# Kernel tuning notes

Hardware: AMD Instinct MI355X
Metric: run time of the kernel (lower is better)

Reference implementation:

```python
import math
import jax, jax.numpy as jnp
import numpy as np

B, T, E = 1, 4096, 768
H, D = 12, 64
RA_WINDOW = 512
INIT_GATES = (2.2, 0.6, 0.1)


def setup_inputs() -> dict:
    key = jax.random.key(0)
    ks = jax.random.split(key, 6)
    x = jax.random.normal(ks[0], (B, T, E), dtype=jnp.float32)
    # Linear weights stored as [in, out] (math-equivalent to torch's x @ W.T)
    s = 1.0 / math.sqrt(E)
    Wq = jax.random.normal(ks[1], (E, H * D), dtype=jnp.float32) * s
    Wk = jax.random.normal(ks[2], (E, H * D), dtype=jnp.float32) * s
    Wv = jax.random.normal(ks[3], (E, H * D), dtype=jnp.float32) * s
    Wo = jax.random.normal(ks[4], (H * D, E), dtype=jnp.float32) * s
    gates = jnp.tile(jnp.asarray(INIT_GATES, dtype=jnp.float32)[None, :], (H, 1))  # [H,3]
    u = jax.random.normal(ks[5], (H, D), dtype=jnp.float32) * 0.02
    return {"x": x, "Wq": Wq, "Wk": Wk, "Wv": Wv, "Wo": Wo, "gates": gates, "u": u}


def reference(x, Wq, Wk, Wv, Wo, gates, u):
    # projections -> [B,H,T,D]
    def proj(W):
        return (x @ W).reshape(B, T, H, D).transpose(0, 2, 1, 3)
    Q, K, V = proj(Wq), proj(Wk), proj(Wv)

    S = jnp.einsum('bhtd,bhsd->bhts', Q, K) / math.sqrt(D)  # [B,H,T,T]

    w = jax.nn.softmax(gates, axis=-1)  # [H,3]
    w_std = w[:, 0][None, :, None, None]
    w_rec = w[:, 1][None, :, None, None]
    w_disc = w[:, 2][None, :, None, None]

    logits = w_std * S + w_rec * jnp.swapaxes(S, -2, -1)

    # discoverability column bias from K via per-head u
    d_raw = jnp.einsum('bhtd,hd->bht', K, u)
    d = d_raw - jnp.mean(d_raw, axis=-1, keepdims=True)
    logits = logits + w_disc * d[:, :, None, :]

    # causal banded mask
    idx = jnp.arange(T)
    mask = (idx[None, :] <= idx[:, None]) & (jnp.abs(idx[None, :] - idx[:, None]) <= RA_WINDOW)
    logits = jnp.where(mask[None, None, :, :], logits, -jnp.inf)

    attn = jax.nn.softmax(logits, axis=-1)
    ctx = jnp.einsum('bhts,bhsd->bhtd', attn, V)
    out = ctx.transpose(0, 2, 1, 3).reshape(B, T, H * D) @ Wo
    return (out, attn)
```

## Files before the change

### kernel.cpp

```cpp
#include <hip/hip_runtime.h>
#include <cstddef>

#define T_LEN 4096
#define EMB 768
#define NH 12
#define HD 64
#define WIN 512
#define PBW 640

#define GBM 128
#define GBN 128
#define GBK 16

__global__ __launch_bounds__(256) void gemm3_f32(const float* __restrict__ A,
                                                 const float* __restrict__ B0,
                                                 const float* __restrict__ B1,
                                                 const float* __restrict__ B2,
                                                 float* __restrict__ C0,
                                                 float* __restrict__ C1,
                                                 float* __restrict__ C2,
                                                 int M, int N, int K) {
    __shared__ float As[GBK][GBM + 4];
    __shared__ float Bs[GBK][GBN + 4];
    const int tid = threadIdx.x;
    const int bm = blockIdx.y * GBM;
    const int bn = blockIdx.x * GBN;
    const float* __restrict__ B = (blockIdx.z == 0) ? B0 : (blockIdx.z == 1) ? B1 : B2;
    float* __restrict__ C = (blockIdx.z == 0) ? C0 : (blockIdx.z == 1) ? C1 : C2;

    const int ty = (tid >> 4) << 2;
    const int tx = (tid & 15) << 2;

    const int ar = tid >> 1;
    const int ac = (tid & 1) << 3;
    const int br = tid >> 4;
    const int bc = (tid & 15) << 3;

    float acc[8][8] = {};

    float4 pa0 = *(const float4*)&A[(size_t)(bm + ar) * K + ac];
    float4 pa1 = *(const float4*)&A[(size_t)(bm + ar) * K + ac + 4];
    float4 pb0 = *(const float4*)&B[(size_t)br * N + bn + bc];
    float4 pb1 = *(const float4*)&B[(size_t)br * N + bn + bc + 4];

    for (int k0 = 0; k0 < K; k0 += GBK) {
        As[ac + 0][ar] = pa0.x; As[ac + 1][ar] = pa0.y; As[ac + 2][ar] = pa0.z; As[ac + 3][ar] = pa0.w;
        As[ac + 4][ar] = pa1.x; As[ac + 5][ar] = pa1.y; As[ac + 6][ar] = pa1.z; As[ac + 7][ar] = pa1.w;
        *(float4*)&Bs[br][bc]     = pb0;
        *(float4*)&Bs[br][bc + 4] = pb1;
        __syncthreads();
        if (k0 + GBK < K) {
            pa0 = *(const float4*)&A[(size_t)(bm + ar) * K + k0 + GBK + ac];
            pa1 = *(const float4*)&A[(size_t)(bm + ar) * K + k0 + GBK + ac + 4];
            pb0 = *(const float4*)&B[(size_t)(k0 + GBK + br) * N + bn + bc];
            pb1 = *(const float4*)&B[(size_t)(k0 + GBK + br) * N + bn + bc + 4];
        }
#pragma unroll
        for (int k = 0; k < GBK; ++k) {
            const float4 a0v = *(const float4*)&As[k][ty];
            const float4 a1v = *(const float4*)&As[k][ty + 64];
            const float4 b0v = *(const float4*)&Bs[k][tx];
            const float4 b1v = *(const float4*)&Bs[k][tx + 64];
            const float av[8] = {a0v.x, a0v.y, a0v.z, a0v.w, a1v.x, a1v.y, a1v.z, a1v.w};
            const float bv[8] = {b0v.x, b0v.y, b0v.z, b0v.w, b1v.x, b1v.y, b1v.z, b1v.w};
#pragma unroll
            for (int i = 0; i < 8; ++i)
#pragma unroll
                for (int j = 0; j < 8; ++j)
                    acc[i][j] += av[i] * bv[j];
        }
        __syncthreads();
    }
#pragma unroll
    for (int i = 0; i < 8; ++i) {
        const int r = bm + ty + ((i < 4) ? i : (60 + i));
        *(float4*)&C[(size_t)r * N + bn + tx]      = make_float4(acc[i][0], acc[i][1], acc[i][2], acc[i][3]);
        *(float4*)&C[(size_t)r * N + bn + tx + 64] = make_float4(acc[i][4], acc[i][5], acc[i][6], acc[i][7]);
    }
}

__global__ __launch_bounds__(256) void dbias_kernel(const float* __restrict__ K,
                                                    const float* __restrict__ u,
                                                    float* __restrict__ d_bias) {
    const int h = blockIdx.x;
    const int tid = threadIdx.x;
    __shared__ __align__(16) float us[HD];
    __shared__ float dr[T_LEN];
    __shared__ float red[256];
    if (tid < HD) us[tid] = u[h * HD + tid];
    __syncthreads();
    const float4* u4 = (const float4*)us;
    float lsum = 0.f;
    for (int t = tid; t < T_LEN; t += 256) {
        const float4* Kp = (const float4*)&K[(size_t)t * EMB + h * HD];
        float acc = 0.f;
#pragma unroll
        for (int i = 0; i < HD / 4; ++i) {
            float4 k4 = Kp[i];
            float4 uu = u4[i];
            acc += k4.x * uu.x + k4.y * uu.y + k4.z * uu.z + k4.w * uu.w;
        }
        dr[t] = acc;
        lsum += acc;
    }
    red[tid] = lsum;
    __syncthreads();
    for (int off = 128; off > 0; off >>= 1) {
        if (tid < off) red[tid] += red[tid + off];
        __syncthreads();
    }
    const float mean = red[0] * (1.0f / (float)T_LEN);
    __syncthreads();
    for (int t = tid; t < T_LEN; t += 256) {
        d_bias[h * T_LEN + t] = dr[t] - mean;
    }
}

__global__ __launch_bounds__(256) void attn_band_kernel(const float* __restrict__ Q,
                                                        const float* __restrict__ K,
                                                        const float* __restrict__ V,
                                                        const float* __restrict__ d_bias,
                                                        const float* __restrict__ gates,
                                                        float* __restrict__ Pb,
                                                        float* __restrict__ Fb,
                                                        float* __restrict__ ctx) {
    const int t0  = blockIdx.x << 6;
    const int h   = blockIdx.y;
    const int tid = threadIdx.x;
    const int cg  = tid & 15;
    const int tm  = (tid >> 4) << 2;
    const int tn4 = cg << 2;

    const int lm = tid >> 2;
    const int lk = (tid & 3) << 4;
    const int sr = tid >> 1;
    const int sc = (tid & 1) << 5;

    __shared__ __align__(16) float QT[64][68];
    __shared__ __align__(16) float KT[64][68];
    __shared__ __align__(16) float Bc[64][136];
    __shared__ float cmf[5][64];
    __shared__ float rmf[64], idvf[64];
    float* __restrict__ Bp = &Bc[0][0];

    const float g0 = gates[h * 3 + 0];
    const float g1 = gates[h * 3 + 1];
    const float g2 = gates[h * 3 + 2];
    const float gm = fmaxf(g0, fmaxf(g1, g2));
    const float e0 = __expf(g0 - gm), e1 = __expf(g1 - gm), e2 = __expf(g2 - gm);
    const float gi = 1.0f / (e0 + e1 + e2);
    const float w_std = e0 * gi * 0.125f;
    const float w_rec = e1 * gi * 0.125f;
    const float w_disc = e2 * gi;

    const int cp_start = (t0 >= 576) ? 0 : ((576 - t0) >> 7);
    int s0 = t0 - 576 + (cp_start << 7);

    float4 kr[8], qr[8];
    {
        int srow = s0 + sr; srow = srow < 0 ? 0 : srow;
        const float* Kp = K + (size_t)srow * EMB + h * HD + sc;
#pragma unroll
        for (int c = 0; c < 8; ++c) kr[c] = *(const float4*)(Kp + 4 * c);
    }

    {
        const float* Qp = Q + (size_t)(t0 + lm) * EMB + h * HD + lk;
        const float* Kp = K + (size_t)(t0 + lm) * EMB + h * HD + lk;
#pragma unroll
        for (int it = 0; it < 4; ++it) {
            float4 a = *(const float4*)(Qp + 4 * it);
            QT[lk + 4 * it + 0][lm] = a.x;
            QT[lk + 4 * it + 1][lm] = a.y;
            QT[lk + 4 * it + 2][lm] = a.z;
            QT[lk + 4 * it + 3][lm] = a.w;
            float4 b = *(const float4*)(Kp + 4 * it);
            KT[lk + 4 * it + 0][lm] = b.x;
            KT[lk + 4 * it + 1][lm] = b.y;
            KT[lk + 4 * it + 2][lm] = b.z;
            KT[lk + 4 * it + 3][lm] = b.w;
        }
    }

    float rm[4], rden[4], acc[4][4];
#pragma unroll
    for (int i = 0; i < 4; ++i) {
        rm[i] = -1e30f;
        rden[i] = 0.f;
#pragma unroll
        for (int j = 0; j < 4; ++j) acc[i][j] = 0.f;
    }

    for (int cp = cp_start; cp < 5; ++cp) {
        __syncthreads();
#pragma unroll
        for (int c = 0; c < 8; ++c) {
            Bc[sc + 4 * c + 0][sr] = kr[c].x;
            Bc[sc + 4 * c + 1][sr] = kr[c].y;
            Bc[sc + 4 * c + 2][sr] = kr[c].z;
            Bc[sc + 4 * c + 3][sr] = kr[c].w;
        }
        __syncthreads();

        {
            int srow = s0 + sr; srow = srow < 0 ? 0 : srow;
            const float* Qp = Q + (size_t)srow * EMB + h * HD + sc;
#pragma unroll
            for (int c = 0; c < 8; ++c) qr[c] = *(const float4*)(Qp + 4 * c);
        }

        float m1[4][8] = {};
#pragma unroll 8
        for (int k = 0; k < 64; ++k) {
            const float4 a4 = *(const float4*)&QT[k][tm];
            const float4 b0 = *(const float4*)&Bc[k][tn4];
            const float4 b1 = *(const float4*)&Bc[k][tn4 + 64];
            const float av[4] = {a4.x, a4.y, a4.z, a4.w};
            const float bv[8] = {b0.x, b0.y, b0.z, b0.w, b1.x, b1.y, b1.z, b1.w};
#pragma unroll
            for (int i = 0; i < 4; ++i)
#pragma unroll
                for (int j = 0; j < 8; ++j)
                    m1[i][j] += av[i] * bv[j];
        }
        __syncthreads();

#pragma unroll
        for (int c = 0; c < 8; ++c) {
            Bc[sc + 4 * c + 0][sr] = qr[c].x;
            Bc[sc + 4 * c + 1][sr] = qr[c].y;
            Bc[sc + 4 * c + 2][sr] = qr[c].z;
            Bc[sc + 4 * c + 3][sr] = qr[c].w;
        }
        __syncthreads();

        if (cp < 4) {
            int srow = s0 + 128 + sr; srow = srow < 0 ? 0 : srow;
            const float* Kp = K + (size_t)srow * EMB + h * HD + sc;
#pragma unroll
            for (int c = 0; c < 8; ++c) kr[c] = *(const float4*)(Kp + 4 * c);
        }

        float m2[4][8] = {};
#pragma unroll 8
        for (int k = 0; k < 64; ++k) {
            const float4 a4 = *(const float4*)&KT[k][tm];
            const float4 b0 = *(const float4*)&Bc[k][tn4];
            const float4 b1 = *(const float4*)&Bc[k][tn4 + 64];
            const float av[4] = {a4.x, a4.y, a4.z, a4.w};
            const float bv[8] = {b0.x, b0.y, b0.z, b0.w, b1.x, b1.y, b1.z, b1.w};
#pragma unroll
            for (int i = 0; i < 4; ++i)
#pragma unroll
                for (int j = 0; j < 8; ++j)
                    m2[i][j] += av[i] * bv[j];
        }

        const int i0 = s0 + tn4;
        const int i0c = i0 < 0 ? 0 : i0;
        const float4 db0 = *(const float4*)&d_bias[h * T_LEN + i0c];
        const float4 db1 = *(const float4*)&d_bias[h * T_LEN + s0 + 64 + tn4];
        const float dbv[8] = {db0.x, db0.y, db0.z, db0.w, db1.x, db1.y, db1.z, db1.w};
        float l[4][8];
#pragma unroll
        for (int i = 0; i < 4; ++i) {
            const int t = t0 + tm + i;
#pragma unroll
            for (int j = 0; j < 8; ++j) {
                const int s = s0 + ((j < 4) ? (tn4 + j) : (tn4 + j + 60));
                const float lv = w_std * m1[i][j] + w_rec * m2[i][j] + w_disc * dbv[j];
                const bool valid = (s >= 0) && (s <= t) && (s >= t - WIN);
                l[i][j] = valid ? lv : -1e30f;
            }
        }
#pragma unroll
        for (int i = 0; i < 4; ++i) {
            float cmx = fmaxf(fmaxf(fmaxf(l[i][0], l[i][1]), fmaxf(l[i][2], l[i][3])),
                              fmaxf(fmaxf(l[i][4], l[i][5]), fmaxf(l[i][6], l[i][7])));
#pragma unroll
            for (int off = 1; off < 16; off <<= 1) cmx = fmaxf(cmx, __shfl_xor(cmx, off));
            const float nm = fmaxf(rm[i], cmx);
            const float f = __expf(rm[i] - nm);
            float cs = 0.f;
#pragma unroll
            for (int j = 0; j < 8; ++j) {
                const float p = __expf(l[i][j] - nm);
                l[i][j] = p;
                cs += p;
            }
#pragma unroll
            for (int off = 1; off < 16; off <<= 1) cs += __shfl_xor(cs, off);
            rden[i] = rden[i] * f + cs;
            rm[i] = nm;
#pragma unroll
            for (int j = 0; j < 4; ++j) acc[i][j] *= f;
            if (cg == 0) cmf[cp][tm + i] = nm;
            float* prow = &Pb[((size_t)(h * T_LEN + t0 + tm + i)) * PBW + (cp << 7)];
            *(float4*)&prow[tn4]      = make_float4(l[i][0], l[i][1], l[i][2], l[i][3]);
            *(float4*)&prow[64 + tn4] = make_float4(l[i][4], l[i][5], l[i][6], l[i][7]);
        }
        __syncthreads();

#pragma unroll
        for (int j = 0; j < 4; ++j) {
            *(float4*)&Bp[(tn4 + j) * 68 + tm] =
                make_float4(l[0][j], l[1][j], l[2][j], l[3][j]);
            *(float4*)&Bp[(tn4 + j + 64) * 68 + tm] =
                make_float4(l[0][j + 4], l[1][j + 4], l[2][j + 4], l[3][j + 4]);
        }
        __syncthreads();

#pragma unroll 8
        for (int k = 0; k < 128; ++k) {
            const float4 av = *(const float4*)&Bp[k * 68 + tm];
            int vrow = s0 + k; vrow = vrow < 0 ? 0 : vrow;
            const float4 bv = *(const float4*)&V[(size_t)vrow * EMB + h * HD + tn4];
            acc[0][0] += av.x * bv.x; acc[0][1] += av.x * bv.y; acc[0][2] += av.x * bv.z; acc[0][3] += av.x * bv.w;
            acc[1][0] += av.y * bv.x; acc[1][1] += av.y * bv.y; acc[1][2] += av.y * bv.z; acc[1][3] += av.y * bv.w;
            acc[2][0] += av.z * bv.x; acc[2][1] += av.z * bv.y; acc[2][2] += av.z * bv.z; acc[2][3] += av.z * bv.w;
            acc[3][0] += av.w * bv.x; acc[3][1] += av.w * bv.y; acc[3][2] += av.w * bv.z; acc[3][3] += av.w * bv.w;
        }
        s0 += 128;
    }

    float idv[4];
#pragma unroll
    for (int i = 0; i < 4; ++i) {
        idv[i] = 1.0f / rden[i];
        *(float4*)&ctx[(size_t)(t0 + tm + i) * EMB + h * HD + tn4] =
            make_float4(acc[i][0] * idv[i], acc[i][1] * idv[i], acc[i][2] * idv[i], acc[i][3] * idv[i]);
    }
    if (cg == 0) {
#pragma unroll
        for (int i = 0; i < 4; ++i) {
            rmf[tm + i] = rm[i];
            idvf[tm + i] = idv[i];
        }
    }
    __syncthreads();
    for (int idx = tid; idx < 320; idx += 256) {
        const int c = idx >> 6, r = idx & 63;
        const float fct = (c >= cp_start) ? __expf(cmf[c][r] - rmf[r]) * idvf[r] : 0.f;
        Fb[((size_t)(h * T_LEN + t0 + r)) * 5 + c] = fct;
    }
}

__global__ __launch_bounds__(256) void attn_expand_kernel(const float* __restrict__ Pb,
                                                          const float* __restrict__ Fb,
                                                          float* __restrict__ attn) {
    const int t = blockIdx.x;
    const int h = blockIdx.y;
    const int base = (t & ~63) - 576;
    const float* prow = Pb + ((size_t)(h * T_LEN + t)) * PBW;
    const float* frow = Fb + ((size_t)(h * T_LEN + t)) * 5;
    float f[5];
#pragma unroll
    for (int c = 0; c < 5; ++c) f[c] = frow[c];
    float* arow = attn + ((size_t)(h * T_LEN + t)) * T_LEN;
    for (int i4 = threadIdx.x << 2; i4 < T_LEN; i4 += 1024) {
        const int j = i4 - base;
        float4 v = make_float4(0.f, 0.f, 0.f, 0.f);
        if (j >= 0 && j < PBW) {
            const float4 p = *(const float4*)&prow[j];
            const float ff = f[j >> 7];
            v = make_float4(p.x * ff, p.y * ff, p.z * ff, p.w * ff);
        }
        *(float4*)&arow[i4] = v;
    }
}

extern "C" void kernel_launch(void* const* d_in, const int* in_sizes, int n_in,
                              void* d_out, int out_size, void* d_ws, size_t ws_size,
                              hipStream_t stream) {
    const float* x     = (const float*)d_in[0];
    const float* Wq    = (const float*)d_in[1];
    const float* Wk    = (const float*)d_in[2];
    const float* Wv    = (const float*)d_in[3];
    const float* Wo    = (const float*)d_in[4];
    const float* gates = (const float*)d_in[5];
    const float* u     = (const float*)d_in[6];

    float* out  = (float*)d_out;
    float* attn = out + (size_t)T_LEN * EMB;

    float* ws = (float*)d_ws;
    float* Qb = ws;
    float* Kb = Qb + (size_t)T_LEN * EMB;
    float* Vb = Kb + (size_t)T_LEN * EMB;
    float* Cb = Vb + (size_t)T_LEN * EMB;
    float* Db = Cb + (size_t)T_LEN * EMB;
    float* Pb = Db + (size_t)NH * T_LEN;
    float* Fb = Pb + (size_t)NH * T_LEN * PBW;

    gemm3_f32<<<dim3(EMB / GBN, T_LEN / GBM, 3), 256, 0, stream>>>(
        x, Wq, Wk, Wv, Qb, Kb, Vb, T_LEN, EMB, EMB);
    dbias_kernel<<<NH, 256, 0, stream>>>(Kb, u, Db);

    attn_band_kernel<<<dim3(T_LEN / 64, NH), 256, 0, stream>>>(Qb, Kb, Vb, Db, gates,
                                                               Pb, Fb, Cb);
    attn_expand_kernel<<<dim3(T_LEN, NH), 256, 0, stream>>>(Pb, Fb, attn);

    gemm3_f32<<<dim3(EMB / GBN, T_LEN / GBM, 1), 256, 0, stream>>>(
        Cb, Wo, Wo, Wo, out, out, out, T_LEN, EMB, EMB);
}
```

Measured before the change: 1.448 ms.

## Fuse attention zero-fill into QKV GEMM and band expansion into Wo GEMM

Zeroing of the out-of-band attention region moves into extra blocks of the QKV projection launch, so that it overlaps the GEMM. The band-only expansion of Pb into attn runs as extra blocks inside the Wo projection launch. The expand path now writes only the 640-wide band instead of whole 4096-wide rows, and the GEMMs are specialised to the fixed EMB size. This removes one launch, overlaps the large memory-bound zero-fill with compute, and writes each attn element once. Correctness depends on the zero-fill and band regions exactly tiling every row, and mixing GEMM blocks with memory blocks in one grid can cause imbalance.

```diff
diff --git a/kernel.cpp b/kernel.cpp
--- a/kernel.cpp
+++ b/kernel.cpp
@@ -12,21 +12,12 @@
 #define GBN 128
 #define GBK 16
 
-__global__ __launch_bounds__(256) void gemm3_f32(const float* __restrict__ A,
-                                                 const float* __restrict__ B0,
-                                                 const float* __restrict__ B1,
-                                                 const float* __restrict__ B2,
-                                                 float* __restrict__ C0,
-                                                 float* __restrict__ C1,
-                                                 float* __restrict__ C2,
-                                                 int M, int N, int K) {
+__device__ __forceinline__ void gemm_128(const float* __restrict__ A,
+                                         const float* __restrict__ B,
+                                         float* __restrict__ C,
+                                         int bm, int bn, int tid) {
     __shared__ float As[GBK][GBM + 4];
     __shared__ float Bs[GBK][GBN + 4];
-    const int tid = threadIdx.x;
-    const int bm = blockIdx.y * GBM;
-    const int bn = blockIdx.x * GBN;
-    const float* __restrict__ B = (blockIdx.z == 0) ? B0 : (blockIdx.z == 1) ? B1 : B2;
-    float* __restrict__ C = (blockIdx.z == 0) ? C0 : (blockIdx.z == 1) ? C1 : C2;
 
     const int ty = (tid >> 4) << 2;
     const int tx = (tid & 15) << 2;
@@ -38,22 +29,22 @@
 
     float acc[8][8] = {};
 
-    float4 pa0 = *(const float4*)&A[(size_t)(bm + ar) * K + ac];
-    float4 pa1 = *(const float4*)&A[(size_t)(bm + ar) * K + ac + 4];
-    float4 pb0 = *(const float4*)&B[(size_t)br * N + bn + bc];
-    float4 pb1 = *(const float4*)&B[(size_t)br * N + bn + bc + 4];
-
-    for (int k0 = 0; k0 < K; k0 += GBK) {
+    float4 pa0 = *(const float4*)&A[(size_t)(bm + ar) * EMB + ac];
+    float4 pa1 = *(const float4*)&A[(size_t)(bm + ar) * EMB + ac + 4];
+    float4 pb0 = *(const float4*)&B[(size_t)br * EMB + bn + bc];
+    float4 pb1 = *(const float4*)&B[(size_t)br * EMB + bn + bc + 4];
+
+    for (int k0 = 0; k0 < EMB; k0 += GBK) {
         As[ac + 0][ar] = pa0.x; As[ac + 1][ar] = pa0.y; As[ac + 2][ar] = pa0.z; As[ac + 3][ar] = pa0.w;
         As[ac + 4][ar] = pa1.x; As[ac + 5][ar] = pa1.y; As[ac + 6][ar] = pa1.z; As[ac + 7][ar] = pa1.w;
         *(float4*)&Bs[br][bc]     = pb0;
         *(float4*)&Bs[br][bc + 4] = pb1;
         __syncthreads();
-        if (k0 + GBK < K) {
-            pa0 = *(const float4*)&A[(size_t)(bm + ar) * K + k0 + GBK + ac];
-            pa1 = *(const float4*)&A[(size_t)(bm + ar) * K + k0 + GBK + ac + 4];
-            pb0 = *(const float4*)&B[(size_t)(k0 + GBK + br) * N + bn + bc];
-            pb1 = *(const float4*)&B[(size_t)(k0 + GBK + br) * N + bn + bc + 4];
+        if (k0 + GBK < EMB) {
+            pa0 = *(const float4*)&A[(size_t)(bm + ar) * EMB + k0 + GBK + ac];
+            pa1 = *(const float4*)&A[(size_t)(bm + ar) * EMB + k0 + GBK + ac + 4];
+            pb0 = *(const float4*)&B[(size_t)(k0 + GBK + br) * EMB + bn + bc];
+            pb1 = *(const float4*)&B[(size_t)(k0 + GBK + br) * EMB + bn + bc + 4];
         }
 #pragma unroll
         for (int k = 0; k < GBK; ++k) {
@@ -74,8 +65,48 @@
 #pragma unroll
     for (int i = 0; i < 8; ++i) {
         const int r = bm + ty + ((i < 4) ? i : (60 + i));
-        *(float4*)&C[(size_t)r * N + bn + tx]      = make_float4(acc[i][0], acc[i][1], acc[i][2], acc[i][3]);
-        *(float4*)&C[(size_t)r * N + bn + tx + 64] = make_float4(acc[i][4], acc[i][5], acc[i][6], acc[i][7]);
+        *(float4*)&C[(size_t)r * EMB + bn + tx]      = make_float4(acc[i][0], acc[i][1], acc[i][2], acc[i][3]);
+        *(float4*)&C[(size_t)r * EMB + bn + tx + 64] = make_float4(acc[i][4], acc[i][5], acc[i][6], acc[i][7]);
+    }
+}
+
+__global__ __launch_bounds__(256) void qkv_zero_kernel(const float* __restrict__ x,
+                                                       const float* __restrict__ Wq,
+                                                       const float* __restrict__ Wk,
+                                                       const float* __restrict__ Wv,
+                                                       float* __restrict__ Qb,
+                                                       float* __restrict__ Kb,
+                                                       float* __restrict__ Vb,
+                                                       float* __restrict__ attn) {
+    const int bid = blockIdx.x;
+    const int tid = threadIdx.x;
+    if (bid < 576) {
+        const int z = bid / 192;
+        const int r = bid % 192;
+        const int bm = (r / 6) * GBM;
+        const int bn = (r % 6) * GBN;
+        const float* B = (z == 0) ? Wq : (z == 1) ? Wk : Wv;
+        float* C = (z == 0) ? Qb : (z == 1) ? Kb : Vb;
+        gemm_128(x, B, C, bm, bn, tid);
+    } else {
+        const int zb = bid - 576;
+        const int rr0 = tid >> 6;
+        const int ln = tid & 63;
+        const float4 z4 = make_float4(0.f, 0.f, 0.f, 0.f);
+        for (int k = 0; k < 4; ++k) {
+            const int p = zb + 192 * k;
+            const int h = p % NH;
+            const int t0 = (p / NH) << 6;
+            const int bl = (t0 >= 576) ? (t0 - 576) : 0;
+            const int br = t0 + 64;
+            for (int rr = rr0; rr < 64; rr += 4) {
+                float* arow = attn + ((size_t)(h * T_LEN + t0 + rr)) * T_LEN;
+                for (int c = ln << 2; c < bl; c += 256)
+                    *(float4*)&arow[c] = z4;
+                for (int c = br + (ln << 2); c < T_LEN; c += 256)
+                    *(float4*)&arow[c] = z4;
+            }
+        }
     }
 }
 
@@ -345,27 +376,35 @@
     }
 }
 
-__global__ __launch_bounds__(256) void attn_expand_kernel(const float* __restrict__ Pb,
-                                                          const float* __restrict__ Fb,
-                                                          float* __restrict__ attn) {
-    const int t = blockIdx.x;
-    const int h = blockIdx.y;
-    const int base = (t & ~63) - 576;
-    const float* prow = Pb + ((size_t)(h * T_LEN + t)) * PBW;
-    const float* frow = Fb + ((size_t)(h * T_LEN + t)) * 5;
-    float f[5];
-#pragma unroll
-    for (int c = 0; c < 5; ++c) f[c] = frow[c];
-    float* arow = attn + ((size_t)(h * T_LEN + t)) * T_LEN;
-    for (int i4 = threadIdx.x << 2; i4 < T_LEN; i4 += 1024) {
-        const int j = i4 - base;
-        float4 v = make_float4(0.f, 0.f, 0.f, 0.f);
-        if (j >= 0 && j < PBW) {
-            const float4 p = *(const float4*)&prow[j];
-            const float ff = f[j >> 7];
-            v = make_float4(p.x * ff, p.y * ff, p.z * ff, p.w * ff);
-        }
-        *(float4*)&arow[i4] = v;
+__global__ __launch_bounds__(256) void wo_expand_kernel(const float* __restrict__ Cb,
+                                                        const float* __restrict__ Wo,
+                                                        float* __restrict__ out,
+                                                        const float* __restrict__ Pb,
+                                                        const float* __restrict__ Fb,
+                                                        float* __restrict__ attn) {
+    const int bid = blockIdx.x;
+    const int tid = threadIdx.x;
+    if (bid < 192) {
+        const int bm = (bid / 6) * GBM;
+        const int bn = (bid % 6) * GBN;
+        gemm_128(Cb, Wo, out, bm, bn, tid);
+    } else {
+        const int e = bid - 192;
+        const int h = e / 1024;
+        const int t = ((e % 1024) << 2) + (tid >> 6);
+        const int ln = tid & 63;
+        const int base = (t & ~63) - 576;
+        const int j_lo = (base < 0) ? -base : 0;
+        const float* prow = Pb + ((size_t)(h * T_LEN + t)) * PBW;
+        const float* frow = Fb + ((size_t)(h * T_LEN + t)) * 5;
+        const float f0 = frow[0], f1 = frow[1], f2 = frow[2], f3 = frow[3], f4 = frow[4];
+        float* arow = attn + ((size_t)(h * T_LEN + t)) * T_LEN;
+        for (int j4 = j_lo + (ln << 2); j4 < PBW; j4 += 256) {
+            const float4 p = *(const float4*)&prow[j4];
+            const float ff = (j4 < 128) ? f0 : (j4 < 256) ? f1 : (j4 < 384) ? f2
+                           : (j4 < 512) ? f3 : f4;
+            *(float4*)&arow[base + j4] = make_float4(p.x * ff, p.y * ff, p.z * ff, p.w * ff);
+        }
     }
 }
 
@@ -392,14 +431,11 @@
     float* Pb = Db + (size_t)NH * T_LEN;
     float* Fb = Pb + (size_t)NH * T_LEN * PBW;
 
-    gemm3_f32<<<dim3(EMB / GBN, T_LEN / GBM, 3), 256, 0, stream>>>(
-        x, Wq, Wk, Wv, Qb, Kb, Vb, T_LEN, EMB, EMB);
+    qkv_zero_kernel<<<768, 256, 0, stream>>>(x, Wq, Wk, Wv, Qb, Kb, Vb, attn);
     dbias_kernel<<<NH, 256, 0, stream>>>(Kb, u, Db);
 
     attn_band_kernel<<<dim3(T_LEN / 64, NH), 256, 0, stream>>>(Qb, Kb, Vb, Db, gates,
                                                                Pb, Fb, Cb);
-    attn_expand_kernel<<<dim3(T_LEN, NH), 256, 0, stream>>>(Pb, Fb, attn);
-
-    gemm3_f32<<<dim3(EMB / GBN, T_LEN / GBM, 1), 256, 0, stream>>>(
-        Cb, Wo, Wo, Wo, out, out, out, T_LEN, EMB, EMB);
-}
+
+    wo_expand_kernel<<<192 + 12288, 256, 0, stream>>>(Cb, Wo, out, Pb, Fb, attn);
+}
```

Result: faster. 1.404 ms (-3.0%).
